# Kernel optimization log

Measured on AMD Instinct MI355X. Metric: run time of the kernel, lower is better.

The kernel has to match this reference:

```python
import jax, jax.numpy as jnp
import numpy as np

B, N = 256, 4096
IMG_W, IMG_H = 640.0, 480.0


def setup_inputs() -> dict:
    key = jax.random.key(0)
    k0, k1, k2, k3 = jax.random.split(key, 4)
    kpts0 = jax.random.uniform(k0, (B, N, 2), dtype=jnp.float32) * jnp.array([IMG_W, IMG_H], jnp.float32)
    kpts1 = jax.random.uniform(k1, (B, N, 2), dtype=jnp.float32) * jnp.array([IMG_W, IMG_H], jnp.float32)
    conf = jax.random.uniform(k2, (B, N, 1), dtype=jnp.float32)
    t_scale = jax.random.uniform(k3, (B, 2), dtype=jnp.float32) + 0.5
    Kmat = jnp.array([[500.0, 0.0, 320.0], [0.0, 500.0, 240.0], [0.0, 0.0, 1.0]], jnp.float32)
    K = jnp.tile(Kmat[None, None], (B, 2, 1, 1))
    gt_pose_0to1 = jnp.tile(jnp.eye(4, dtype=jnp.float32)[None], (B, 1, 1))
    return {"kpts0": kpts0, "kpts1": kpts1, "conf": conf, "t_scale": t_scale, "K": K, "gt_pose_0to1": gt_pose_0to1}


def _normalize(kpts, Kmat):
    # pixel -> normalized camera coords, homogeneous. kpts:[B,N,2], Kmat:[B,3,3] -> [B,N,3]
    Kinv = jnp.linalg.inv(Kmat)
    h = jnp.concatenate([kpts, jnp.ones_like(kpts[..., :1])], axis=-1)
    return jnp.einsum('bij,bnj->bni', Kinv, h)


def _se3_weighted_8pt(kpts0, kpts1, K0, K1, w, t_scale):
    b_, n_ = kpts0.shape[0], kpts0.shape[1]
    x0 = _normalize(kpts0, K0)  # [B,N,3]
    x1 = _normalize(kpts1, K1)  # [B,N,3]
    # epipolar constraint x1^T E x0 = 0 -> row kron(x1, x0): [B,N,9]
    X = (x1[..., :, None] * x0[..., None, :]).reshape(b_, n_, 9)
    # confidence-weighted normal equations, 9x9 per batch
    M = jnp.einsum('bn,bni,bnj->bij', w, X, X)
    _, V = jnp.linalg.eigh(M)
    E = V[..., 0].reshape(b_, 3, 3)  # eigvec of smallest eigenvalue
    # project to essential manifold + decompose
    U, S, Vt = jnp.linalg.svd(E)
    W = jnp.array([[0.0, -1.0, 0.0], [1.0, 0.0, 0.0], [0.0, 0.0, 1.0]], E.dtype)
    R1 = U @ W @ Vt
    R2 = U @ W.T @ Vt
    R1 = R1 * jnp.sign(jnp.linalg.det(R1))[:, None, None]
    R2 = R2 * jnp.sign(jnp.linalg.det(R2))[:, None, None]
    t = U[..., 2]  # [B,3]
    Rc = jnp.stack([R1, R1, R2, R2], axis=1)   # [B,4,3,3]
    tc = jnp.stack([t, -t, t, -t], axis=1)     # [B,4,3]
    # cheirality: solve d0 * (R x0) - d1 * x1 = -t in least squares (2x2 closed form)
    a = jnp.einsum('bcij,bnj->bcni', Rc, x0)   # [B,4,N,3]
    bvec = x1[:, None]                          # [B,1,N,3]
    tt = tc[:, :, None, :]                      # [B,4,1,3]
    aa = jnp.sum(a * a, -1)
    bb = jnp.sum(bvec * bvec, -1)
    ab = jnp.sum(a * bvec, -1)
    at = jnp.sum(a * tt, -1)
    bt = jnp.sum(bvec * tt, -1)
    det = aa * bb - ab * ab + 1e-9
    d0 = (-at * bb + ab * bt) / det
    d1 = (aa * bt - ab * at) / det
    pos = ((d0 > 0) & (d1 > 0)).astype(w.dtype)
    score = jnp.sum(w[:, None] * pos, -1)       # [B,4]
    best = jnp.argmax(jax.lax.stop_gradient(score), axis=-1)
    oh = jax.nn.one_hot(best, 4, dtype=kpts0.dtype)
    R = jnp.einsum('bc,bcij->bij', oh, Rc)
    t_best = jnp.einsum('bc,bci->bi', oh, tc)
    t_sc = t_best * t_scale[:, None]            # scale unit translation
    top = jnp.concatenate([R, t_sc[..., None]], axis=-1)  # [B,3,4]
    bot = jnp.broadcast_to(jnp.array([0.0, 0.0, 0.0, 1.0], R.dtype), (b_, 1, 4))
    return jnp.concatenate([top, bot], axis=1)  # [B,4,4]


def _se3_inverse(T):
    R = T[:, :3, :3]
    t = T[:, :3, 3:]
    Rt = jnp.swapaxes(R, -1, -2)
    tin = -(Rt @ t)
    top = jnp.concatenate([Rt, tin], axis=-1)
    bot = jnp.broadcast_to(jnp.array([0.0, 0.0, 0.0, 1.0], T.dtype), (T.shape[0], 1, 4))
    return jnp.concatenate([top, bot], axis=1)


def reference(kpts0, kpts1, conf, t_scale, K, gt_pose_0to1):
    w = conf[..., 0]
    T01 = _se3_weighted_8pt(kpts0, kpts1, K[:, 0], K[:, 1], w, t_scale[:, 0])
    T10 = _se3_inverse(T01)
    return jnp.stack([T01, T10], axis=1)  # [B,2,4,4]
```

## Files before the change

### kernel.cpp

```cpp
#include <hip/hip_runtime.h>
#include <math.h>

#define NBATCH 256
#define NPTS   4096
#define NT     512
#define PPT    (NPTS / NT)
#define NWAVE  (NT / 64)

#define IDX(r,c)   ((r)*((r)+1)/2+(c))
#define UPIDX(r,c) ((r)*9 - ((r)*((r)-1))/2 + ((c)-(r)))

__device__ __forceinline__ void inv3x3f(const float* __restrict__ Km, float* Ki) {
  double a = Km[0], bb = Km[1], c = Km[2];
  double d = Km[3], e  = Km[4], f = Km[5];
  double g = Km[6], h  = Km[7], i = Km[8];
  double C00 =  e*i - f*h;
  double C01 = -(d*i - f*g);
  double C02 =  d*h - e*g;
  double det = a*C00 + bb*C01 + c*C02;
  double rd = 1.0/det;
  Ki[0] = (float)(C00*rd); Ki[1] = (float)(-(bb*i - c*h)*rd); Ki[2] = (float)( (bb*f - c*e)*rd);
  Ki[3] = (float)(C01*rd); Ki[4] = (float)( (a*i  - c*g)*rd); Ki[5] = (float)(-(a*f  - c*d)*rd);
  Ki[6] = (float)(C02*rd); Ki[7] = (float)(-(a*h - bb*g)*rd); Ki[8] = (float)( (a*e  - bb*d)*rd);
}

__global__ __launch_bounds__(NT, 1)
void pose_fused(const float* __restrict__ kpts0,
                const float* __restrict__ kpts1,
                const float* __restrict__ conf,
                const float* __restrict__ t_scale,
                const float* __restrict__ Kmat,
                float* __restrict__ out)
{
  const int b    = blockIdx.x;
  const int tid  = threadIdx.x;
  const int lane = tid & 63;
  const int wv   = tid >> 6;

  __shared__ float  red[NWAVE][45];
  __shared__ double sMd[45];
  __shared__ float  sR[21];
  __shared__ float  sscore[NWAVE][4];

  float Ki0[9], Ki1[9];
  inv3x3f(Kmat + (size_t)b*18,     Ki0);
  inv3x3f(Kmat + (size_t)b*18 + 9, Ki1);

  const float4* k0p4 = (const float4*)(kpts0 + (size_t)b*NPTS*2);
  const float4* k1p4 = (const float4*)(kpts1 + (size_t)b*NPTS*2);
  const float2* cp2  = (const float2*)(conf  + (size_t)b*NPTS);

  float px0[PPT][3], px1[PPT][3], pw[PPT];
  float acc[45];
#pragma unroll
  for (int j=0;j<45;j++) acc[j] = 0.f;

#pragma unroll
  for (int p=0;p<PPT/2;p++) {
    const int idx = tid + p*NT;
    const float4 q0 = k0p4[idx];
    const float4 q1 = k1p4[idx];
    const float2 w2 = cp2[idx];
#pragma unroll
    for (int h=0; h<2; h++) {
      const int pt = 2*p + h;
      const float u0 = h ? q0.z : q0.x, v0 = h ? q0.w : q0.y;
      const float u1 = h ? q1.z : q1.x, v1 = h ? q1.w : q1.y;
      const float w  = h ? w2.y : w2.x;
      float x0[3], x1[3];
      x0[0] = fmaf(Ki0[0],u0, fmaf(Ki0[1],v0, Ki0[2]));
      x0[1] = fmaf(Ki0[3],u0, fmaf(Ki0[4],v0, Ki0[5]));
      x0[2] = fmaf(Ki0[6],u0, fmaf(Ki0[7],v0, Ki0[8]));
      x1[0] = fmaf(Ki1[0],u1, fmaf(Ki1[1],v1, Ki1[2]));
      x1[1] = fmaf(Ki1[3],u1, fmaf(Ki1[4],v1, Ki1[5]));
      x1[2] = fmaf(Ki1[6],u1, fmaf(Ki1[7],v1, Ki1[8]));
#pragma unroll
      for (int j=0;j<3;j++) { px0[pt][j] = x0[j]; px1[pt][j] = x1[j]; }
      pw[pt] = w;
      float X[9], wX[9];
#pragma unroll
      for (int ii=0; ii<3; ii++)
#pragma unroll
        for (int jj=0; jj<3; jj++)
          X[ii*3+jj] = x1[ii]*x0[jj];
#pragma unroll
      for (int j=0;j<9;j++) wX[j] = w*X[j];
      int k = 0;
#pragma unroll
      for (int r=0;r<9;r++)
#pragma unroll
        for (int c=r;c<9;c++) { acc[k] = fmaf(wX[r], X[c], acc[k]); k++; }
    }
  }

#pragma unroll
  for (int j=0;j<45;j++) {
    float v = acc[j];
#pragma unroll
    for (int off=32; off>0; off>>=1) v += __shfl_xor(v, off, 64);
    acc[j] = v;
  }
  if (lane == 0) {
#pragma unroll
    for (int j=0;j<45;j++) red[wv][j] = acc[j];
  }
  __syncthreads();
  if (tid < 45) {
    double s = 0.0;
#pragma unroll
    for (int wq=0; wq<NWAVE; wq++) s += (double)red[wq][tid];
    sMd[tid] = s;
  }
  __syncthreads();

  if (tid == 0) {
    double L[45];
#pragma unroll
    for (int r=0;r<9;r++)
#pragma unroll
      for (int c=0;c<=r;c++)
        L[IDX(r,c)] = sMd[UPIDX(c,r)];

    double dinv[9];
#pragma unroll
    for (int k=0;k<9;k++) {
      double s = L[IDX(k,k)];
#pragma unroll
      for (int j=0;j<k;j++) s -= L[IDX(k,j)]*L[IDX(k,j)];
      double l = sqrt(fmax(s, 1e-30));
      L[IDX(k,k)] = l;
      dinv[k] = 1.0/l;
#pragma unroll
      for (int i2=k+1;i2<9;i2++) {
        double s2 = L[IDX(i2,k)];
#pragma unroll
        for (int j=0;j<k;j++) s2 -= L[IDX(i2,j)]*L[IDX(k,j)];
        L[IDX(i2,k)] = s2*dinv[k];
      }
    }

#pragma unroll
    for (int j=0;j<9;j++) {
#pragma unroll
      for (int i2=j+1;i2<9;i2++) {
        double s = L[IDX(i2,j)]*dinv[j];
#pragma unroll
        for (int k=j+1;k<i2;k++) s += L[IDX(i2,k)]*L[IDX(k,j)];
        L[IDX(i2,j)] = -s*dinv[i2];
      }
    }
#pragma unroll
    for (int j=0;j<9;j++) L[IDX(j,j)] = dinv[j];

#pragma unroll
    for (int i2=0;i2<9;i2++) {
      double tmp[9];
#pragma unroll
      for (int j=0;j<=i2;j++) {
        double s = 0.0;
#pragma unroll
        for (int k=i2;k<9;k++) s += L[IDX(k,i2)]*L[IDX(k,j)];
        tmp[j] = s;
      }
#pragma unroll
      for (int j=0;j<=i2;j++) L[IDX(i2,j)] = tmp[j];
    }

    double v[9];
#pragma unroll
    for (int j=0;j<9;j++) v[j] = 0.125;
    v[4] = 1.0;
    for (int it=0; it<20; it++) {
      double y[9];
#pragma unroll
      for (int i2=0;i2<9;i2++) {
        double s = 0.0;
#pragma unroll
        for (int j=0;j<9;j++) {
          const int rr = (i2>j)?i2:j, cc = (i2>j)?j:i2;
          s = fma(L[IDX(rr,cc)], v[j], s);
        }
        y[i2] = s;
      }
#pragma unroll
      for (int j=0;j<9;j++) v[j] = y[j];
    }
    {
      double nn = 0.0;
#pragma unroll
      for (int j=0;j<9;j++) nn += v[j]*v[j];
      double rn = 1.0/sqrt(nn);
#pragma unroll
      for (int j=0;j<9;j++) v[j] *= rn;
    }

    double E0[3][3];
#pragma unroll
    for (int ii=0;ii<3;ii++)
#pragma unroll
      for (int jj=0;jj<3;jj++) E0[ii][jj] = v[ii*3+jj];
    double G[3][3];
#pragma unroll
    for (int a2=0;a2<3;a2++)
#pragma unroll
      for (int b2=0;b2<3;b2++)
        G[a2][b2] = E0[0][a2]*E0[0][b2] + E0[1][a2]*E0[1][b2] + E0[2][a2]*E0[2][b2];
    double Vv[3][3] = {{1,0,0},{0,1,0},{0,0,1}};
#define JROT(P,Q,RR) do { \
      double apq = G[P][Q]; \
      if (fabs(apq) > 1e-300) { \
        double app = G[P][P], aqq = G[Q][Q]; \
        double tau = (aqq - app) / (2.0*apq); \
        double tt = ((tau >= 0.0) ? 1.0 : -1.0) / (fabs(tau) + sqrt(1.0 + tau*tau)); \
        double cc_ = 1.0/sqrt(1.0 + tt*tt); \
        double ss_ = tt*cc_; \
        G[P][P] = app - tt*apq; \
        G[Q][Q] = aqq + tt*apq; \
        G[P][Q] = 0.0; G[Q][P] = 0.0; \
        double grp = G[RR][P], grq = G[RR][Q]; \
        G[RR][P] = cc_*grp - ss_*grq; G[P][RR] = G[RR][P]; \
        G[RR][Q] = ss_*grp + cc_*grq; G[Q][RR] = G[RR][Q]; \
        double v0p = Vv[0][P], v0q = Vv[0][Q]; \
        Vv[0][P] = cc_*v0p - ss_*v0q; Vv[0][Q] = ss_*v0p + cc_*v0q; \
        double v1p = Vv[1][P], v1q = Vv[1][Q]; \
        Vv[1][P] = cc_*v1p - ss_*v1q; Vv[1][Q] = ss_*v1p + cc_*v1q; \
        double v2p = Vv[2][P], v2q = Vv[2][Q]; \
        Vv[2][P] = cc_*v2p - ss_*v2q; Vv[2][Q] = ss_*v2p + cc_*v2q; \
      } } while(0)
    for (int sw=0; sw<6; sw++) { JROT(0,1,2); JROT(0,2,1); JROT(1,2,0); }
#undef JROT
    double lam[3] = {G[0][0], G[1][1], G[2][2]};
#define CSWAP(A_,B_) if (lam[A_] < lam[B_]) { \
      double tl = lam[A_]; lam[A_] = lam[B_]; lam[B_] = tl; \
      double t0_ = Vv[0][A_]; Vv[0][A_] = Vv[0][B_]; Vv[0][B_] = t0_; \
      double t1_ = Vv[1][A_]; Vv[1][A_] = Vv[1][B_]; Vv[1][B_] = t1_; \
      double t2_ = Vv[2][A_]; Vv[2][A_] = Vv[2][B_]; Vv[2][B_] = t2_; }
    CSWAP(0,1); CSWAP(0,2); CSWAP(1,2);
#undef CSWAP
    double u1[3], u2[3], u3[3];
#pragma unroll
    for (int i3=0;i3<3;i3++)
      u1[i3] = E0[i3][0]*Vv[0][0] + E0[i3][1]*Vv[1][0] + E0[i3][2]*Vv[2][0];
    double n1 = 1.0/sqrt(fmax(u1[0]*u1[0]+u1[1]*u1[1]+u1[2]*u1[2], 1e-300));
#pragma unroll
    for (int i3=0;i3<3;i3++) u1[i3] *= n1;
#pragma unroll
    for (int i3=0;i3<3;i3++)
      u2[i3] = E0[i3][0]*Vv[0][1] + E0[i3][1]*Vv[1][1] + E0[i3][2]*Vv[2][1];
    double d12 = u1[0]*u2[0]+u1[1]*u2[1]+u1[2]*u2[2];
#pragma unroll
    for (int i3=0;i3<3;i3++) u2[i3] -= d12*u1[i3];
    double n2 = 1.0/sqrt(fmax(u2[0]*u2[0]+u2[1]*u2[1]+u2[2]*u2[2], 1e-300));
#pragma unroll
    for (int i3=0;i3<3;i3++) u2[i3] *= n2;
    u3[0] = u1[1]*u2[2] - u1[2]*u2[1];
    u3[1] = u1[2]*u2[0] - u1[0]*u2[2];
    u3[2] = u1[0]*u2[1] - u1[1]*u2[0];
    double R1a[9], R2a[9];
#pragma unroll
    for (int i3=0;i3<3;i3++)
#pragma unroll
      for (int j3=0;j3<3;j3++) {
        double m  = u3[i3]*Vv[j3][2];
        double pA = u2[i3]*Vv[j3][0] - u1[i3]*Vv[j3][1];
        R1a[i3*3+j3] = pA + m;
        R2a[i3*3+j3] = m - pA;
      }
    double det1 = R1a[0]*(R1a[4]*R1a[8]-R1a[5]*R1a[7])
                - R1a[1]*(R1a[3]*R1a[8]-R1a[5]*R1a[6])
                + R1a[2]*(R1a[3]*R1a[7]-R1a[4]*R1a[6]);
    double det2 = R2a[0]*(R2a[4]*R2a[8]-R2a[5]*R2a[7])
                - R2a[1]*(R2a[3]*R2a[8]-R2a[5]*R2a[6])
                + R2a[2]*(R2a[3]*R2a[7]-R2a[4]*R2a[6]);
    double sg1 = (det1 < 0.0) ? -1.0 : 1.0;
    double sg2 = (det2 < 0.0) ? -1.0 : 1.0;
#pragma unroll
    for (int j3=0;j3<9;j3++) { sR[j3] = (float)(sg1*R1a[j3]); sR[9+j3] = (float)(sg2*R2a[j3]); }
    sR[18] = (float)u3[0]; sR[19] = (float)u3[1]; sR[20] = (float)u3[2];
  }
  __syncthreads();

  float r1[9], r2[9], tv[3];
#pragma unroll
  for (int j=0;j<9;j++) { r1[j] = sR[j]; r2[j] = sR[9+j]; }
  tv[0] = sR[18]; tv[1] = sR[19]; tv[2] = sR[20];

  float sc[4] = {0.f, 0.f, 0.f, 0.f};
#pragma unroll
  for (int p=0;p<PPT;p++) {
    const float x00 = px0[p][0], x01 = px0[p][1], x02 = px0[p][2];
    const float x10 = px1[p][0], x11 = px1[p][1], x12 = px1[p][2];
    const float w   = pw[p];
    const float bb2 = x10*x10 + x11*x11 + x12*x12;
    const float bt  = x10*tv[0] + x11*tv[1] + x12*tv[2];
    {
      float a0 = r1[0]*x00 + r1[1]*x01 + r1[2]*x02;
      float a1 = r1[3]*x00 + r1[4]*x01 + r1[5]*x02;
      float a2 = r1[6]*x00 + r1[7]*x01 + r1[8]*x02;
      float aa = a0*a0 + a1*a1 + a2*a2;
      float ab = a0*x10 + a1*x11 + a2*x12;
      float at = a0*tv[0] + a1*tv[1] + a2*tv[2];
      float n0v = ab*bt - at*bb2;
      float n1v = aa*bt - ab*at;
      if (n0v > 0.f && n1v > 0.f) sc[0] += w;
      if (n0v < 0.f && n1v < 0.f) sc[1] += w;
    }
    {
      float a0 = r2[0]*x00 + r2[1]*x01 + r2[2]*x02;
      float a1 = r2[3]*x00 + r2[4]*x01 + r2[5]*x02;
      float a2 = r2[6]*x00 + r2[7]*x01 + r2[8]*x02;
      float aa = a0*a0 + a1*a1 + a2*a2;
      float ab = a0*x10 + a1*x11 + a2*x12;
      float at = a0*tv[0] + a1*tv[1] + a2*tv[2];
      float n0v = ab*bt - at*bb2;
      float n1v = aa*bt - ab*at;
      if (n0v > 0.f && n1v > 0.f) sc[2] += w;
      if (n0v < 0.f && n1v < 0.f) sc[3] += w;
    }
  }
#pragma unroll
  for (int c=0;c<4;c++) {
    float vv = sc[c];
#pragma unroll
    for (int off=32; off>0; off>>=1) vv += __shfl_xor(vv, off, 64);
    sc[c] = vv;
  }
  if (lane == 0) {
#pragma unroll
    for (int c=0;c<4;c++) sscore[wv][c] = sc[c];
  }
  __syncthreads();

  if (tid == 0) {
    float st[4];
#pragma unroll
    for (int c=0;c<4;c++) {
      float s = 0.f;
#pragma unroll
      for (int wq=0; wq<NWAVE; wq++) s += sscore[wq][c];
      st[c] = s;
    }
    int bestc = 0; float bs = st[0];
    if (st[1] > bs) { bs = st[1]; bestc = 1; }
    if (st[2] > bs) { bs = st[2]; bestc = 2; }
    if (st[3] > bs) { bs = st[3]; bestc = 3; }
    float Rb[9];
#pragma unroll
    for (int j=0;j<9;j++) Rb[j] = (bestc < 2) ? r1[j] : r2[j];
    const float sg = (bestc & 1) ? -1.f : 1.f;
    const float ts = t_scale[(size_t)b*2];
    const float t0 = sg*tv[0]*ts, t1 = sg*tv[1]*ts, t2 = sg*tv[2]*ts;
    float* o = out + (size_t)b*32;
    o[0]=Rb[0]; o[1]=Rb[1]; o[2] =Rb[2]; o[3] =t0;
    o[4]=Rb[3]; o[5]=Rb[4]; o[6] =Rb[5]; o[7] =t1;
    o[8]=Rb[6]; o[9]=Rb[7]; o[10]=Rb[8]; o[11]=t2;
    o[12]=0.f; o[13]=0.f; o[14]=0.f; o[15]=1.f;
    const float ti0 = -(Rb[0]*t0 + Rb[3]*t1 + Rb[6]*t2);
    const float ti1 = -(Rb[1]*t0 + Rb[4]*t1 + Rb[7]*t2);
    const float ti2 = -(Rb[2]*t0 + Rb[5]*t1 + Rb[8]*t2);
    o[16]=Rb[0]; o[17]=Rb[3]; o[18]=Rb[6]; o[19]=ti0;
    o[20]=Rb[1]; o[21]=Rb[4]; o[22]=Rb[7]; o[23]=ti1;
    o[24]=Rb[2]; o[25]=Rb[5]; o[26]=Rb[8]; o[27]=ti2;
    o[28]=0.f; o[29]=0.f; o[30]=0.f; o[31]=1.f;
  }
}

extern "C" void kernel_launch(void* const* d_in, const int* in_sizes, int n_in,
                              void* d_out, int out_size, void* d_ws, size_t ws_size,
                              hipStream_t stream) {
  (void)in_sizes; (void)n_in; (void)out_size; (void)d_ws; (void)ws_size;
  const float* kpts0  = (const float*)d_in[0];
  const float* kpts1  = (const float*)d_in[1];
  const float* conf   = (const float*)d_in[2];
  const float* tscale = (const float*)d_in[3];
  const float* K      = (const float*)d_in[4];
  float* outp = (float*)d_out;
  pose_fused<<<dim3(NBATCH), dim3(NT), 0, stream>>>(kpts0, kpts1, conf, tscale, K, outp);
}
```

Baseline: 98.11 us.

## Parallelize triangular inverse and power iteration across lanes of one wave

Keeps the Cholesky factorization on one lane but spreads the triangular inverse, the M^-1 formation and the 20-step power iteration across 9 lanes of wave 0, using LDS and shuffles to share the vector. This shortens the serial single-thread double-precision tail that every block runs between the reduction and the cheirality pass. It relies on wave-level LDS ordering via s_waitcnt plus sched_barrier instead of __syncthreads, and it adds shared-memory traffic.

```diff
diff --git a/kernel.cpp b/kernel.cpp
--- a/kernel.cpp
+++ b/kernel.cpp
@@ -39,6 +39,9 @@
 
   __shared__ float  red[NWAVE][45];
   __shared__ double sMd[45];
+  __shared__ double sLp[45];
+  __shared__ double sDinv[9];
+  __shared__ double sW[81];
   __shared__ float  sR[21];
   __shared__ float  sscore[NWAVE][4];
 
@@ -113,99 +116,112 @@
   }
   __syncthreads();
 
-  if (tid == 0) {
-    double L[45];
-#pragma unroll
-    for (int r=0;r<9;r++)
-#pragma unroll
-      for (int c=0;c<=r;c++)
-        L[IDX(r,c)] = sMd[UPIDX(c,r)];
-
-    double dinv[9];
-#pragma unroll
-    for (int k=0;k<9;k++) {
-      double s = L[IDX(k,k)];
-#pragma unroll
-      for (int j=0;j<k;j++) s -= L[IDX(k,j)]*L[IDX(k,j)];
-      double l = sqrt(fmax(s, 1e-30));
-      L[IDX(k,k)] = l;
-      dinv[k] = 1.0/l;
-#pragma unroll
-      for (int i2=k+1;i2<9;i2++) {
-        double s2 = L[IDX(i2,k)];
-#pragma unroll
-        for (int j=0;j<k;j++) s2 -= L[IDX(i2,j)]*L[IDX(k,j)];
-        L[IDX(i2,k)] = s2*dinv[k];
-      }
-    }
-
-#pragma unroll
-    for (int j=0;j<9;j++) {
-#pragma unroll
-      for (int i2=j+1;i2<9;i2++) {
-        double s = L[IDX(i2,j)]*dinv[j];
-#pragma unroll
-        for (int k=j+1;k<i2;k++) s += L[IDX(i2,k)]*L[IDX(k,j)];
-        L[IDX(i2,j)] = -s*dinv[i2];
-      }
-    }
-#pragma unroll
-    for (int j=0;j<9;j++) L[IDX(j,j)] = dinv[j];
-
-#pragma unroll
-    for (int i2=0;i2<9;i2++) {
-      double tmp[9];
-#pragma unroll
-      for (int j=0;j<=i2;j++) {
+  if (wv == 0) {
+    if (lane == 0) {
+      double L[45];
+#pragma unroll
+      for (int r=0;r<9;r++)
+#pragma unroll
+        for (int c=0;c<=r;c++)
+          L[IDX(r,c)] = sMd[UPIDX(c,r)];
+
+      double dinv[9];
+#pragma unroll
+      for (int k=0;k<9;k++) {
+        double s = L[IDX(k,k)];
+#pragma unroll
+        for (int j=0;j<k;j++) s -= L[IDX(k,j)]*L[IDX(k,j)];
+        double l = sqrt(fmax(s, 1e-30));
+        L[IDX(k,k)] = l;
+        dinv[k] = 1.0/l;
+#pragma unroll
+        for (int i2=k+1;i2<9;i2++) {
+          double s2 = L[IDX(i2,k)];
+#pragma unroll
+          for (int j=0;j<k;j++) s2 -= L[IDX(i2,j)]*L[IDX(k,j)];
+          L[IDX(i2,k)] = s2*dinv[k];
+        }
+      }
+#pragma unroll
+      for (int j=0;j<45;j++) sLp[j] = L[j];
+#pragma unroll
+      for (int k=0;k<9;k++) sDinv[k] = dinv[k];
+    }
+    asm volatile("s_waitcnt lgkmcnt(0)" ::: "memory");
+    __builtin_amdgcn_sched_barrier(0);
+
+    double vlan[9];
+    if (lane < 9) {
+      const double dj = sDinv[lane];
+      double cw[9];
+#pragma unroll
+      for (int i=0;i<9;i++) cw[i] = (i == lane) ? dj : 0.0;
+#pragma unroll
+      for (int i2=1;i2<9;i2++) {
         double s = 0.0;
 #pragma unroll
-        for (int k=i2;k<9;k++) s += L[IDX(k,i2)]*L[IDX(k,j)];
-        tmp[j] = s;
-      }
-#pragma unroll
-      for (int j=0;j<=i2;j++) L[IDX(i2,j)] = tmp[j];
-    }
-
-    double v[9];
-#pragma unroll
-    for (int j=0;j<9;j++) v[j] = 0.125;
-    v[4] = 1.0;
-    for (int it=0; it<20; it++) {
-      double y[9];
-#pragma unroll
-      for (int i2=0;i2<9;i2++) {
+        for (int k=0;k<i2;k++) s = fma(sLp[IDX(i2,k)], cw[k], s);
+        const double ci2 = -s*sDinv[i2];
+        cw[i2] = (i2 > lane) ? ci2 : cw[i2];
+      }
+#pragma unroll
+      for (int k=0;k<9;k++) sW[k*9 + lane] = cw[k];
+    }
+    asm volatile("s_waitcnt lgkmcnt(0)" ::: "memory");
+    __builtin_amdgcn_sched_barrier(0);
+
+    if (lane < 9) {
+      double wcol[9], Brow[9];
+#pragma unroll
+      for (int k=0;k<9;k++) wcol[k] = sW[k*9 + lane];
+#pragma unroll
+      for (int j=0;j<9;j++) {
         double s = 0.0;
 #pragma unroll
-        for (int j=0;j<9;j++) {
-          const int rr = (i2>j)?i2:j, cc = (i2>j)?j:i2;
-          s = fma(L[IDX(rr,cc)], v[j], s);
-        }
-        y[i2] = s;
-      }
-#pragma unroll
-      for (int j=0;j<9;j++) v[j] = y[j];
-    }
-    {
-      double nn = 0.0;
-#pragma unroll
-      for (int j=0;j<9;j++) nn += v[j]*v[j];
-      double rn = 1.0/sqrt(nn);
-#pragma unroll
-      for (int j=0;j<9;j++) v[j] *= rn;
-    }
-
-    double E0[3][3];
-#pragma unroll
-    for (int ii=0;ii<3;ii++)
-#pragma unroll
-      for (int jj=0;jj<3;jj++) E0[ii][jj] = v[ii*3+jj];
-    double G[3][3];
-#pragma unroll
-    for (int a2=0;a2<3;a2++)
-#pragma unroll
-      for (int b2=0;b2<3;b2++)
-        G[a2][b2] = E0[0][a2]*E0[0][b2] + E0[1][a2]*E0[1][b2] + E0[2][a2]*E0[2][b2];
-    double Vv[3][3] = {{1,0,0},{0,1,0},{0,0,1}};
+        for (int k=0;k<9;k++) s = fma(wcol[k], sW[k*9 + j], s);
+        Brow[j] = s;
+      }
+
+      double vv[9];
+#pragma unroll
+      for (int j=0;j<9;j++) vv[j] = 0.125;
+      vv[4] = 1.0;
+      for (int it=0; it<20; ++it) {
+        double y = 0.0;
+#pragma unroll
+        for (int j=0;j<9;j++) y = fma(Brow[j], vv[j], y);
+#pragma unroll
+        for (int j=0;j<9;j++) vv[j] = __shfl(y, j, 64);
+      }
+#pragma unroll
+      for (int j=0;j<9;j++) vlan[j] = vv[j];
+    }
+
+    if (lane == 0) {
+      double v[9];
+#pragma unroll
+      for (int j=0;j<9;j++) v[j] = vlan[j];
+      {
+        double nn = 0.0;
+#pragma unroll
+        for (int j=0;j<9;j++) nn += v[j]*v[j];
+        double rn = 1.0/sqrt(nn);
+#pragma unroll
+        for (int j=0;j<9;j++) v[j] *= rn;
+      }
+
+      double E0[3][3];
+#pragma unroll
+      for (int ii=0;ii<3;ii++)
+#pragma unroll
+        for (int jj=0;jj<3;jj++) E0[ii][jj] = v[ii*3+jj];
+      double G[3][3];
+#pragma unroll
+      for (int a2=0;a2<3;a2++)
+#pragma unroll
+        for (int b2=0;b2<3;b2++)
+          G[a2][b2] = E0[0][a2]*E0[0][b2] + E0[1][a2]*E0[1][b2] + E0[2][a2]*E0[2][b2];
+      double Vv[3][3] = {{1,0,0},{0,1,0},{0,0,1}};
 #define JROT(P,Q,RR) do { \
       double apq = G[P][Q]; \
       if (fabs(apq) > 1e-300) { \
@@ -227,56 +243,57 @@
         double v2p = Vv[2][P], v2q = Vv[2][Q]; \
         Vv[2][P] = cc_*v2p - ss_*v2q; Vv[2][Q] = ss_*v2p + cc_*v2q; \
       } } while(0)
-    for (int sw=0; sw<6; sw++) { JROT(0,1,2); JROT(0,2,1); JROT(1,2,0); }
+      for (int sw=0; sw<6; sw++) { JROT(0,1,2); JROT(0,2,1); JROT(1,2,0); }
 #undef JROT
-    double lam[3] = {G[0][0], G[1][1], G[2][2]};
+      double lam[3] = {G[0][0], G[1][1], G[2][2]};
 #define CSWAP(A_,B_) if (lam[A_] < lam[B_]) { \
       double tl = lam[A_]; lam[A_] = lam[B_]; lam[B_] = tl; \
       double t0_ = Vv[0][A_]; Vv[0][A_] = Vv[0][B_]; Vv[0][B_] = t0_; \
       double t1_ = Vv[1][A_]; Vv[1][A_] = Vv[1][B_]; Vv[1][B_] = t1_; \
       double t2_ = Vv[2][A_]; Vv[2][A_] = Vv[2][B_]; Vv[2][B_] = t2_; }
-    CSWAP(0,1); CSWAP(0,2); CSWAP(1,2);
+      CSWAP(0,1); CSWAP(0,2); CSWAP(1,2);
 #undef CSWAP
-    double u1[3], u2[3], u3[3];
-#pragma unroll
-    for (int i3=0;i3<3;i3++)
-      u1[i3] = E0[i3][0]*Vv[0][0] + E0[i3][1]*Vv[1][0] + E0[i3][2]*Vv[2][0];
-    double n1 = 1.0/sqrt(fmax(u1[0]*u1[0]+u1[1]*u1[1]+u1[2]*u1[2], 1e-300));
-#pragma unroll
-    for (int i3=0;i3<3;i3++) u1[i3] *= n1;
-#pragma unroll
-    for (int i3=0;i3<3;i3++)
-      u2[i3] = E0[i3][0]*Vv[0][1] + E0[i3][1]*Vv[1][1] + E0[i3][2]*Vv[2][1];
-    double d12 = u1[0]*u2[0]+u1[1]*u2[1]+u1[2]*u2[2];
-#pragma unroll
-    for (int i3=0;i3<3;i3++) u2[i3] -= d12*u1[i3];
-    double n2 = 1.0/sqrt(fmax(u2[0]*u2[0]+u2[1]*u2[1]+u2[2]*u2[2], 1e-300));
-#pragma unroll
-    for (int i3=0;i3<3;i3++) u2[i3] *= n2;
-    u3[0] = u1[1]*u2[2] - u1[2]*u2[1];
-    u3[1] = u1[2]*u2[0] - u1[0]*u2[2];
-    u3[2] = u1[0]*u2[1] - u1[1]*u2[0];
-    double R1a[9], R2a[9];
-#pragma unroll
-    for (int i3=0;i3<3;i3++)
-#pragma unroll
-      for (int j3=0;j3<3;j3++) {
-        double m  = u3[i3]*Vv[j3][2];
-        double pA = u2[i3]*Vv[j3][0] - u1[i3]*Vv[j3][1];
-        R1a[i3*3+j3] = pA + m;
-        R2a[i3*3+j3] = m - pA;
-      }
-    double det1 = R1a[0]*(R1a[4]*R1a[8]-R1a[5]*R1a[7])
-                - R1a[1]*(R1a[3]*R1a[8]-R1a[5]*R1a[6])
-                + R1a[2]*(R1a[3]*R1a[7]-R1a[4]*R1a[6]);
-    double det2 = R2a[0]*(R2a[4]*R2a[8]-R2a[5]*R2a[7])
-                - R2a[1]*(R2a[3]*R2a[8]-R2a[5]*R2a[6])
-                + R2a[2]*(R2a[3]*R2a[7]-R2a[4]*R2a[6]);
-    double sg1 = (det1 < 0.0) ? -1.0 : 1.0;
-    double sg2 = (det2 < 0.0) ? -1.0 : 1.0;
-#pragma unroll
-    for (int j3=0;j3<9;j3++) { sR[j3] = (float)(sg1*R1a[j3]); sR[9+j3] = (float)(sg2*R2a[j3]); }
-    sR[18] = (float)u3[0]; sR[19] = (float)u3[1]; sR[20] = (float)u3[2];
+      double u1[3], u2[3], u3[3];
+#pragma unroll
+      for (int i3=0;i3<3;i3++)
+        u1[i3] = E0[i3][0]*Vv[0][0] + E0[i3][1]*Vv[1][0] + E0[i3][2]*Vv[2][0];
+      double n1 = 1.0/sqrt(fmax(u1[0]*u1[0]+u1[1]*u1[1]+u1[2]*u1[2], 1e-300));
+#pragma unroll
+      for (int i3=0;i3<3;i3++) u1[i3] *= n1;
+#pragma unroll
+      for (int i3=0;i3<3;i3++)
+        u2[i3] = E0[i3][0]*Vv[0][1] + E0[i3][1]*Vv[1][1] + E0[i3][2]*Vv[2][1];
+      double d12 = u1[0]*u2[0]+u1[1]*u2[1]+u1[2]*u2[2];
+#pragma unroll
+      for (int i3=0;i3<3;i3++) u2[i3] -= d12*u1[i3];
+      double n2 = 1.0/sqrt(fmax(u2[0]*u2[0]+u2[1]*u2[1]+u2[2]*u2[2], 1e-300));
+#pragma unroll
+      for (int i3=0;i3<3;i3++) u2[i3] *= n2;
+      u3[0] = u1[1]*u2[2] - u1[2]*u2[1];
+      u3[1] = u1[2]*u2[0] - u1[0]*u2[2];
+      u3[2] = u1[0]*u2[1] - u1[1]*u2[0];
+      double R1a[9], R2a[9];
+#pragma unroll
+      for (int i3=0;i3<3;i3++)
+#pragma unroll
+        for (int j3=0;j3<3;j3++) {
+          double m  = u3[i3]*Vv[j3][2];
+          double pA = u2[i3]*Vv[j3][0] - u1[i3]*Vv[j3][1];
+          R1a[i3*3+j3] = pA + m;
+          R2a[i3*3+j3] = m - pA;
+        }
+      double det1 = R1a[0]*(R1a[4]*R1a[8]-R1a[5]*R1a[7])
+                  - R1a[1]*(R1a[3]*R1a[8]-R1a[5]*R1a[6])
+                  + R1a[2]*(R1a[3]*R1a[7]-R1a[4]*R1a[6]);
+      double det2 = R2a[0]*(R2a[4]*R2a[8]-R2a[5]*R2a[7])
+                  - R2a[1]*(R2a[3]*R2a[8]-R2a[5]*R2a[6])
+                  + R2a[2]*(R2a[3]*R2a[7]-R2a[4]*R2a[6]);
+      double sg1 = (det1 < 0.0) ? -1.0 : 1.0;
+      double sg2 = (det2 < 0.0) ? -1.0 : 1.0;
+#pragma unroll
+      for (int j3=0;j3<9;j3++) { sR[j3] = (float)(sg1*R1a[j3]); sR[9+j3] = (float)(sg2*R2a[j3]); }
+      sR[18] = (float)u3[0]; sR[19] = (float)u3[1]; sR[20] = (float)u3[2];
+    }
   }
   __syncthreads();
 
```

After: 97.04 us. No clear change (-1.1%).
